# Kernel optimization log

Hardware: AMD Instinct MI355X
Metric: run time of the kernel (lower is better)

The kernel has to match this reference:

```python
import jax, jax.numpy as jnp
import numpy as np

N, E = 50000, 400000          # nodes, edges
T, R = 4, 8                   # node types, relations (edge types)
H, DK = 8, 32                 # heads, head dim
DIN = DOUT = 256              # in/out feature dim (DOUT = H*DK)
SQRT_DK = float(np.sqrt(DK))


def setup_inputs() -> dict:
    key = jax.random.key(0)
    ks = jax.random.split(key, 12)
    f32 = jnp.float32
    return {
        "x": jax.random.normal(ks[0], (N, DIN), f32),
        "node_type": jax.random.randint(ks[1], (N,), 0, T, jnp.int32),
        "src": jax.random.randint(ks[2], (E,), 0, N, jnp.int32),
        "dst": jax.random.randint(ks[3], (E,), 0, N, jnp.int32),
        "etype": jax.random.randint(ks[4], (E,), 0, R, jnp.int32),
        "Wk": jax.random.normal(ks[5], (T, DOUT, DIN), f32) / np.sqrt(DIN).astype(np.float32),
        "bk": jnp.zeros((T, DOUT), f32),
        "Wq": jax.random.normal(ks[6], (T, DOUT, DIN), f32) / np.sqrt(DIN).astype(np.float32),
        "bq": jnp.zeros((T, DOUT), f32),
        "Wv": jax.random.normal(ks[7], (T, DOUT, DIN), f32) / np.sqrt(DIN).astype(np.float32),
        "bv": jnp.zeros((T, DOUT), f32),
        "Wa": jax.random.normal(ks[8], (T, DOUT, DOUT), f32) / np.sqrt(DOUT).astype(np.float32),
        "ba": jnp.zeros((T, DOUT), f32),
        "rel_pri": jnp.ones((R, H), f32),
        "rel_att": jax.random.normal(ks[9], (R, H, DK, DK), f32) / np.sqrt(DK).astype(np.float32),  # ~xavier
        "rel_msg": jax.random.normal(ks[10], (R, H, DK, DK), f32) / np.sqrt(DK).astype(np.float32),
        "skip": jnp.ones((T,), f32),
    }


def _typed_linear(h, W, b, ntype):
    # per-node-type linear: y_n = W[type_n] @ h_n + b[type_n]
    y = jnp.einsum('ni,tdi->ntd', h, W)                      # [N,T,D] (T is small)
    y = jnp.take_along_axis(y, ntype[:, None, None], axis=1)[:, 0]
    return y + b[ntype]


def _hgt_forward(x, node_type, src, dst, etype,
                 Wk, bk, Wq, bq, Wv, bv, Wa, ba,
                 rel_pri, rel_att, rel_msg, skip):
    # typed k/q/v projections -> [N,H,DK]
    K = _typed_linear(x, Wk, bk, node_type).reshape(N, H, DK)
    Q = _typed_linear(x, Wq, bq, node_type).reshape(N, H, DK)
    V = _typed_linear(x, Wv, bv, node_type).reshape(N, H, DK)

    k_e, q_e, v_e = K[src], Q[dst], V[src]                   # [E,H,DK] gathers

    # per-relation head transforms (loop over small fixed R, masked accumulate)
    key_e = jnp.zeros_like(k_e)
    msg_e = jnp.zeros_like(v_e)
    for r in range(R):
        m = (etype == r)[:, None, None].astype(x.dtype)
        key_e = key_e + m * jnp.einsum('ehd,hdf->ehf', k_e, rel_att[r])
        msg_e = msg_e + m * jnp.einsum('ehd,hdf->ehf', v_e, rel_msg[r])

    att = (q_e * key_e).sum(-1) * rel_pri[etype] / SQRT_DK   # [E,H]

    # softmax per (dst node, edge type) segment, then mean across edge types
    seg = dst * R + etype                                    # [E]
    S = N * R
    amax = jax.ops.segment_max(att, seg, num_segments=S)     # [S,H]
    ex = jnp.exp(att - amax[seg])
    denom = jax.ops.segment_sum(ex, seg, num_segments=S)
    w = ex / denom[seg]                                      # normalized attention [E,H]
    h_seg = jax.ops.segment_sum(w[:, :, None] * msg_e, seg, num_segments=S)  # [S,H,DK]
    cnt = jax.ops.segment_sum(jnp.ones((E,), x.dtype), seg, num_segments=S)  # [S]

    h_nr = h_seg.reshape(N, R, DOUT)
    present = (cnt.reshape(N, R) > 0).astype(x.dtype)        # which etypes hit each node
    t = h_nr.sum(1) / jnp.maximum(present.sum(1), 1.0)[:, None]  # cross_reducer='mean'

    trans = _typed_linear(t, Wa, ba, node_type)              # per-type output linear
    alpha = jax.nn.sigmoid(skip)[node_type][:, None]
    return trans * alpha + x * (1.0 - alpha)


def reference(x, node_type, src, dst, etype,
              Wk, bk, Wq, bq, Wv, bv, Wa, ba,
              rel_pri, rel_att, rel_msg, skip):
    return _hgt_forward(x, node_type, src, dst, etype,
                        Wk, bk, Wq, bq, Wv, bv, Wa, ba,
                        rel_pri, rel_att, rel_msg, skip)
```

## Files before the change

### kernel.cpp

```cpp
#include <hip/hip_runtime.h>
#include <math.h>
#include <stdint.h>

#define N_NODES 50000
#define N_EDGES 400000
#define N_T 4
#define N_R 8
#define N_H 8
#define DKD 32
#define D 256
#define TM 64
#define N_SEG (N_NODES * N_R)
#define EMASK 0xFFFFF
#define PROJ_BLOCKS ((N_NODES + TM - 1) / TM + N_T)

typedef __bf16 v8bf __attribute__((ext_vector_type(8)));
typedef float v4f __attribute__((ext_vector_type(4)));
typedef unsigned short u16;

__device__ __forceinline__ u16 f2bf(float f) {
    unsigned int u = __float_as_uint(f);
    u += 0x7fffu + ((u >> 16) & 1u);
    return (u16)(u >> 16);
}

__device__ __forceinline__ void load_bf32(const u16* __restrict__ p, float* f) {
    const uint4* p4 = (const uint4*)p;
    #pragma unroll
    for (int j = 0; j < 4; j++) {
        uint4 u = p4[j];
        f[8 * j + 0] = __uint_as_float(u.x << 16);
        f[8 * j + 1] = __uint_as_float(u.x & 0xffff0000u);
        f[8 * j + 2] = __uint_as_float(u.y << 16);
        f[8 * j + 3] = __uint_as_float(u.y & 0xffff0000u);
        f[8 * j + 4] = __uint_as_float(u.z << 16);
        f[8 * j + 5] = __uint_as_float(u.z & 0xffff0000u);
        f[8 * j + 6] = __uint_as_float(u.w << 16);
        f[8 * j + 7] = __uint_as_float(u.w & 0xffff0000u);
    }
}

__device__ __forceinline__ float dot8f(uint4 m, const float* v) {
    float s;
    s  = __uint_as_float(m.x << 16)          * v[0];
    s += __uint_as_float(m.x & 0xffff0000u)  * v[1];
    s += __uint_as_float(m.y << 16)          * v[2];
    s += __uint_as_float(m.y & 0xffff0000u)  * v[3];
    s += __uint_as_float(m.z << 16)          * v[4];
    s += __uint_as_float(m.z & 0xffff0000u)  * v[5];
    s += __uint_as_float(m.w << 16)          * v[6];
    s += __uint_as_float(m.w & 0xffff0000u)  * v[7];
    return s;
}

__global__ __launch_bounds__(256) void k_cvt4(const float4* __restrict__ s,
                                              ushort4* __restrict__ d, int n4) {
    int i = blockIdx.x * 256 + threadIdx.x;
    if (i < n4) {
        float4 v = s[i];
        ushort4 o;
        o.x = f2bf(v.x); o.y = f2bf(v.y); o.z = f2bf(v.z); o.w = f2bf(v.w);
        d[i] = o;
    }
}

__global__ __launch_bounds__(256) void k_cvt_t(const float* __restrict__ s,
                                               u16* __restrict__ d) {
    int i = blockIdx.x * 256 + threadIdx.x;
    if (i >= N_R * N_H * DKD * DKD) return;
    int mat = i >> 10, w = i & 1023;
    int d0 = w >> 5, f = w & 31;
    d[(mat << 10) + f * DKD + d0] = f2bf(s[i]);
}

__global__ void k_hist(const int* __restrict__ nt, int* __restrict__ cnt) {
    int n = blockIdx.x * blockDim.x + threadIdx.x;
    if (n < N_NODES) atomicAdd(&cnt[nt[n]], 1);
}

__global__ void k_scan(const int* __restrict__ cnt, int* __restrict__ off,
                       int* __restrict__ toff) {
    int o = 0, to = 0;
    for (int t = 0; t < N_T; t++) {
        off[t] = o; toff[t] = to;
        o += cnt[t]; to += (cnt[t] + TM - 1) / TM;
    }
    off[N_T] = o; toff[N_T] = to;
}

__global__ void k_scatter(const int* __restrict__ nt, const int* __restrict__ off,
                          int* __restrict__ cur, int* __restrict__ order) {
    int n = blockIdx.x * blockDim.x + threadIdx.x;
    if (n >= N_NODES) return;
    int t = nt[n];
    int pos = off[t] + atomicAdd(&cur[t], 1);
    order[pos] = n;
}

__global__ void k_hist_seg(const int* __restrict__ dst, const int* __restrict__ et,
                           int* __restrict__ cnt) {
    int e = blockIdx.x * blockDim.x + threadIdx.x;
    if (e < N_EDGES) atomicAdd(&cnt[dst[e] * N_R + et[e]], 1);
}

__global__ __launch_bounds__(1024) void k_scan_l1(const int* __restrict__ cnt,
                                                  int* __restrict__ excl,
                                                  int* __restrict__ bsum) {
    __shared__ int sh[1024];
    int tid = threadIdx.x, i = blockIdx.x * 1024 + tid;
    int v = (i < N_SEG) ? cnt[i] : 0;
    sh[tid] = v;
    __syncthreads();
    #pragma unroll
    for (int ofs = 1; ofs < 1024; ofs <<= 1) {
        int t = (tid >= ofs) ? sh[tid - ofs] : 0;
        __syncthreads();
        sh[tid] += t;
        __syncthreads();
    }
    if (i < N_SEG) excl[i] = sh[tid] - v;
    if (tid == 1023) bsum[blockIdx.x] = sh[1023];
}

__global__ __launch_bounds__(512) void k_scan_l2(int* __restrict__ bsum, int NB) {
    __shared__ int sh[512];
    int tid = threadIdx.x;
    int v = (tid < NB) ? bsum[tid] : 0;
    sh[tid] = v;
    __syncthreads();
    #pragma unroll
    for (int ofs = 1; ofs < 512; ofs <<= 1) {
        int t = (tid >= ofs) ? sh[tid - ofs] : 0;
        __syncthreads();
        sh[tid] += t;
        __syncthreads();
    }
    if (tid < NB) bsum[tid] = sh[tid] - v;
}

__global__ void k_scan_l3(int* __restrict__ excl, const int* __restrict__ bsum) {
    int i = blockIdx.x * blockDim.x + threadIdx.x;
    if (i < N_SEG) excl[i] += bsum[i >> 10];
    else if (i == N_SEG) excl[N_SEG] = N_EDGES;
}

__global__ void k_scatter_seg(const int* __restrict__ src, const int* __restrict__ dst,
                              const int* __restrict__ et, const int* __restrict__ rp,
                              int* __restrict__ cur, int* __restrict__ esrc) {
    int e = blockIdx.x * blockDim.x + threadIdx.x;
    if (e >= N_EDGES) return;
    int r = et[e];
    int sg = dst[e] * N_R + r;
    int pos = rp[sg] + atomicAdd(&cur[sg], 1);
    esrc[pos] = src[e] | (r << 20);
}

__global__ __launch_bounds__(256) void k_proj(
    const float* __restrict__ x, const int* __restrict__ order,
    const int* __restrict__ off, const int* __restrict__ toff,
    const u16* __restrict__ Wkb, const float* __restrict__ bk,
    const u16* __restrict__ Wqb, const float* __restrict__ bq,
    const u16* __restrict__ Wvb, const float* __restrict__ bv,
    u16* __restrict__ Kb, u16* __restrict__ Qb, u16* __restrict__ Vb) {
    __shared__ __align__(16) u16 xs[TM][D + 8];
    int b = blockIdx.x;
    int t = -1;
    #pragma unroll
    for (int i = 0; i < N_T; i++)
        if (b >= toff[i] && b < toff[i + 1]) t = i;
    if (t < 0) return;
    int nodeBase = off[t] + (b - toff[t]) * TM;
    int count = min(TM, off[t + 1] - nodeBase);
    int tid = threadIdx.x;

    for (int j = tid; j < TM * (D / 4); j += 256) {
        int row = j >> 6, ch = j & 63;
        float4 v = {0.f, 0.f, 0.f, 0.f};
        if (row < count) {
            int g = order[nodeBase + row];
            v = *(const float4*)(x + (size_t)g * D + ch * 4);
        }
        ushort4 o;
        o.x = f2bf(v.x); o.y = f2bf(v.y); o.z = f2bf(v.z); o.w = f2bf(v.w);
        *(ushort4*)&xs[row][ch * 4] = o;
    }
    __syncthreads();

    int lane = tid & 63, wave = tid >> 6;
    int m = lane & 15, quad = lane >> 4;
    v8bf a[8];
    #pragma unroll
    for (int ks = 0; ks < 8; ks++)
        a[ks] = *(const v8bf*)&xs[wave * 16 + m][ks * 32 + quad * 8];

    int grow[4]; bool vrow[4];
    #pragma unroll
    for (int r = 0; r < 4; r++) {
        int rowi = wave * 16 + quad * 4 + r;
        vrow[r] = (rowi < count);
        grow[r] = vrow[r] ? order[nodeBase + rowi] : 0;
    }

    const u16* Ws[3] = {Wkb + (size_t)t * D * D, Wqb + (size_t)t * D * D, Wvb + (size_t)t * D * D};
    const float* Bs[3] = {bk + t * D, bq + t * D, bv + t * D};
    u16* Os[3] = {Kb, Qb, Vb};

    for (int p = 0; p < 3; p++) {
        const u16* W = Ws[p];
        for (int dt = 0; dt < 16; dt++) {
            int dcol = dt * 16 + m;
            v4f acc = {0.f, 0.f, 0.f, 0.f};
            #pragma unroll
            for (int ks = 0; ks < 8; ks++) {
                v8bf bf = *(const v8bf*)(W + (size_t)dcol * D + ks * 32 + quad * 8);
                acc = __builtin_amdgcn_mfma_f32_16x16x32_bf16(a[ks], bf, acc, 0, 0, 0);
            }
            float bias = Bs[p][dcol];
            #pragma unroll
            for (int r = 0; r < 4; r++) {
                if (vrow[r])
                    Os[p][(size_t)grow[r] * D + dcol] = f2bf(acc[r] + bias);
            }
        }
    }
}

__global__ __launch_bounds__(256) void k_fused(
    const u16* __restrict__ Kb, u16* QTb, const u16* __restrict__ Vb,
    const int* __restrict__ rowptr, const int* __restrict__ esrc,
    const u16* __restrict__ Ab, const u16* __restrict__ Mtb,
    const float* __restrict__ pri) {
    __shared__ __align__(16) float Uld[4][N_H][40];
    int wave = threadIdx.x >> 6, lane = threadIdx.x & 63;
    int n = blockIdx.x * 4 + wave;
    if (n >= N_NODES) return;
    int h = lane >> 3, fo = (lane & 7) * 4;
    int base = n * N_R;

    int bnd[N_R + 1];
    #pragma unroll
    for (int i = 0; i <= N_R; i++) bnd[i] = rowptr[base + i];

    float qv[32];
    load_bf32(QTb + (size_t)n * D + h * DKD, qv);

    float qt[N_R][4];
    int np = 0;
    #pragma unroll
    for (int r = 0; r < N_R; r++) {
        if (bnd[r] >= bnd[r + 1]) continue;
        np++;
        const u16* Ar = Ab + ((size_t)(r * N_H + h) * DKD + fo) * DKD;
        float scale = pri[r * N_H + h] * 0.17677669529663687f;
        #pragma unroll
        for (int i = 0; i < 4; i++) {
            const uint4* ar = (const uint4*)(Ar + i * DKD);
            qt[r][i] = scale * (dot8f(ar[0], qv) + dot8f(ar[1], qv + 8)
                     + dot8f(ar[2], qv + 16) + dot8f(ar[3], qv + 24));
        }
    }

    float den[N_R] = {0.f, 0.f, 0.f, 0.f, 0.f, 0.f, 0.f, 0.f};
    float ua[N_R][4] = {};

#define DOTQ(P, RS, KU) { \
    float _k0 = __uint_as_float((KU).x << 16); \
    float _k1 = __uint_as_float((KU).x & 0xffff0000u); \
    float _k2 = __uint_as_float((KU).y << 16); \
    float _k3 = __uint_as_float((KU).y & 0xffff0000u); \
    switch (RS) { \
    case 0: P = _k0*qt[0][0]+_k1*qt[0][1]+_k2*qt[0][2]+_k3*qt[0][3]; break; \
    case 1: P = _k0*qt[1][0]+_k1*qt[1][1]+_k2*qt[1][2]+_k3*qt[1][3]; break; \
    case 2: P = _k0*qt[2][0]+_k1*qt[2][1]+_k2*qt[2][2]+_k3*qt[2][3]; break; \
    case 3: P = _k0*qt[3][0]+_k1*qt[3][1]+_k2*qt[3][2]+_k3*qt[3][3]; break; \
    case 4: P = _k0*qt[4][0]+_k1*qt[4][1]+_k2*qt[4][2]+_k3*qt[4][3]; break; \
    case 5: P = _k0*qt[5][0]+_k1*qt[5][1]+_k2*qt[5][2]+_k3*qt[5][3]; break; \
    case 6: P = _k0*qt[6][0]+_k1*qt[6][1]+_k2*qt[6][2]+_k3*qt[6][3]; break; \
    default: P = _k0*qt[7][0]+_k1*qt[7][1]+_k2*qt[7][2]+_k3*qt[7][3]; break; } }

#define ACCR(R, EX, V0, V1, V2, V3) \
    den[R] += EX; ua[R][0] += EX*V0; ua[R][1] += EX*V1; ua[R][2] += EX*V2; ua[R][3] += EX*V3;

#define ACCE(RS, EX, VU) { \
    float _v0 = __uint_as_float((VU).x << 16); \
    float _v1 = __uint_as_float((VU).x & 0xffff0000u); \
    float _v2 = __uint_as_float((VU).y << 16); \
    float _v3 = __uint_as_float((VU).y & 0xffff0000u); \
    switch (RS) { \
    case 0: ACCR(0, EX, _v0, _v1, _v2, _v3) break; \
    case 1: ACCR(1, EX, _v0, _v1, _v2, _v3) break; \
    case 2: ACCR(2, EX, _v0, _v1, _v2, _v3) break; \
    case 3: ACCR(3, EX, _v0, _v1, _v2, _v3) break; \
    case 4: ACCR(4, EX, _v0, _v1, _v2, _v3) break; \
    case 5: ACCR(5, EX, _v0, _v1, _v2, _v3) break; \
    case 6: ACCR(6, EX, _v0, _v1, _v2, _v3) break; \
    default: ACCR(7, EX, _v0, _v1, _v2, _v3) break; } }

    int eb = bnd[0], ee = bnd[N_R];
    size_t hoff = (size_t)(h * DKD + fo);
    for (int w0 = eb; w0 < ee; w0 += 64) {
        int wcnt = min(64, ee - w0);
        int myek = (lane < wcnt) ? esrc[w0 + lane] : 0;
        for (int i0 = 0; i0 < wcnt; i0 += 4) {
            int mc = wcnt - i0;
            int pk0 = __shfl(myek, i0);
            int pk1 = __shfl(myek, i0 + (mc > 1 ? 1 : 0));
            int pk2 = __shfl(myek, i0 + (mc > 2 ? 2 : 0));
            int pk3 = __shfl(myek, i0 + (mc > 3 ? 3 : 0));
            int s0 = pk0 & EMASK, s1 = pk1 & EMASK, s2 = pk2 & EMASK, s3 = pk3 & EMASK;
            int r0 = __builtin_amdgcn_readfirstlane(pk0) >> 20;
            int r1 = __builtin_amdgcn_readfirstlane(pk1) >> 20;
            int r2 = __builtin_amdgcn_readfirstlane(pk2) >> 20;
            int r3 = __builtin_amdgcn_readfirstlane(pk3) >> 20;
            uint2 ku0 = *(const uint2*)(Kb + (size_t)s0 * D + hoff);
            uint2 ku1 = *(const uint2*)(Kb + (size_t)s1 * D + hoff);
            uint2 ku2 = *(const uint2*)(Kb + (size_t)s2 * D + hoff);
            uint2 ku3 = *(const uint2*)(Kb + (size_t)s3 * D + hoff);
            uint2 vu0 = *(const uint2*)(Vb + (size_t)s0 * D + hoff);
            uint2 vu1 = *(const uint2*)(Vb + (size_t)s1 * D + hoff);
            uint2 vu2 = *(const uint2*)(Vb + (size_t)s2 * D + hoff);
            uint2 vu3 = *(const uint2*)(Vb + (size_t)s3 * D + hoff);
            float p0, p1, p2, p3;
            DOTQ(p0, r0, ku0);
            DOTQ(p1, r1, ku1);
            DOTQ(p2, r2, ku2);
            DOTQ(p3, r3, ku3);
            p0 += __shfl_xor(p0, 1); p1 += __shfl_xor(p1, 1);
            p2 += __shfl_xor(p2, 1); p3 += __shfl_xor(p3, 1);
            p0 += __shfl_xor(p0, 2); p1 += __shfl_xor(p1, 2);
            p2 += __shfl_xor(p2, 2); p3 += __shfl_xor(p3, 2);
            p0 += __shfl_xor(p0, 4); p1 += __shfl_xor(p1, 4);
            p2 += __shfl_xor(p2, 4); p3 += __shfl_xor(p3, 4);
            float ex0 = __expf(p0), ex1 = __expf(p1);
            float ex2 = __expf(p2), ex3 = __expf(p3);
            ACCE(r0, ex0, vu0);
            if (mc > 1) { ACCE(r1, ex1, vu1); }
            if (mc > 2) { ACCE(r2, ex2, vu2); }
            if (mc > 3) { ACCE(r3, ex3, vu3); }
        }
    }

    float macc[4] = {0.f, 0.f, 0.f, 0.f};
    #pragma unroll
    for (int r = 0; r < N_R; r++) {
        if (bnd[r] >= bnd[r + 1]) continue;
        float invd = 1.f / den[r];
        float4 uw = {ua[r][0] * invd, ua[r][1] * invd, ua[r][2] * invd, ua[r][3] * invd};
        __builtin_amdgcn_wave_barrier();
        *(float4*)&Uld[wave][h][fo] = uw;
        __builtin_amdgcn_wave_barrier();
        float Uv[32];
        #pragma unroll
        for (int i = 0; i < 8; i++)
            *(float4*)&Uv[4 * i] = *(const float4*)&Uld[wave][h][4 * i];
        const u16* mp = Mtb + ((size_t)(r * N_H + h) * DKD + fo) * DKD;
        #pragma unroll
        for (int j = 0; j < 4; j++) {
            const uint4* mr = (const uint4*)(mp + j * DKD);
            macc[j] += dot8f(mr[0], Uv) + dot8f(mr[1], Uv + 8)
                     + dot8f(mr[2], Uv + 16) + dot8f(mr[3], Uv + 24);
        }
        __builtin_amdgcn_wave_barrier();
    }

    float invp = (np > 0) ? 1.f / (float)np : 1.f;
    ushort4 o;
    o.x = f2bf(macc[0] * invp); o.y = f2bf(macc[1] * invp);
    o.z = f2bf(macc[2] * invp); o.w = f2bf(macc[3] * invp);
    *(ushort4*)(QTb + (size_t)n * D + hoff) = o;
}

__global__ __launch_bounds__(256) void k_out(
    const u16* __restrict__ TBF, const float* __restrict__ x,
    const int* __restrict__ order, const int* __restrict__ off, const int* __restrict__ toff,
    const u16* __restrict__ Wab, const float* __restrict__ ba,
    const float* __restrict__ skip, float* __restrict__ out) {
    __shared__ __align__(16) u16 xs[TM][D + 8];
    int b = blockIdx.x;
    int t = -1;
    #pragma unroll
    for (int i = 0; i < N_T; i++)
        if (b >= toff[i] && b < toff[i + 1]) t = i;
    if (t < 0) return;
    int nodeBase = off[t] + (b - toff[t]) * TM;
    int count = min(TM, off[t + 1] - nodeBase);
    int tid = threadIdx.x;

    for (int j = tid; j < TM * 32; j += 256) {
        int row = j >> 5, ch = j & 31;
        ushort4 z = {0, 0, 0, 0};
        if (row < count) {
            int g = order[nodeBase + row];
            const ushort4* p = (const ushort4*)(TBF + (size_t)g * D + ch * 8);
            *(ushort4*)&xs[row][ch * 8] = p[0];
            *(ushort4*)&xs[row][ch * 8 + 4] = p[1];
        } else {
            *(ushort4*)&xs[row][ch * 8] = z;
            *(ushort4*)&xs[row][ch * 8 + 4] = z;
        }
    }
    __syncthreads();

    int lane = tid & 63, wave = tid >> 6;
    int m = lane & 15, quad = lane >> 4;
    v8bf a[8];
    #pragma unroll
    for (int ks = 0; ks < 8; ks++)
        a[ks] = *(const v8bf*)&xs[wave * 16 + m][ks * 32 + quad * 8];

    int grow[4]; bool vrow[4];
    #pragma unroll
    for (int r = 0; r < 4; r++) {
        int rowi = wave * 16 + quad * 4 + r;
        vrow[r] = (rowi < count);
        grow[r] = vrow[r] ? order[nodeBase + rowi] : 0;
    }

    float sv = skip[t];
    float alpha = 1.f / (1.f + __expf(-sv));
    float beta = 1.f - alpha;
    const u16* W = Wab + (size_t)t * D * D;

    for (int dt = 0; dt < 16; dt++) {
        int dcol = dt * 16 + m;
        v4f acc = {0.f, 0.f, 0.f, 0.f};
        #pragma unroll
        for (int ks = 0; ks < 8; ks++) {
            v8bf bf = *(const v8bf*)(W + (size_t)dcol * D + ks * 32 + quad * 8);
            acc = __builtin_amdgcn_mfma_f32_16x16x32_bf16(a[ks], bf, acc, 0, 0, 0);
        }
        float bias = ba[t * D + dcol];
        #pragma unroll
        for (int r = 0; r < 4; r++) {
            if (vrow[r]) {
                size_t o = (size_t)grow[r] * D + dcol;
                out[o] = alpha * (acc[r] + bias) + beta * x[o];
            }
        }
    }
}

extern "C" void kernel_launch(void* const* d_in, const int* in_sizes, int n_in,
                              void* d_out, int out_size, void* d_ws, size_t ws_size,
                              hipStream_t stream) {
    const float* x       = (const float*)d_in[0];
    const int* node_type = (const int*)d_in[1];
    const int* src       = (const int*)d_in[2];
    const int* dst       = (const int*)d_in[3];
    const int* etype     = (const int*)d_in[4];
    const float* Wk = (const float*)d_in[5];
    const float* bk = (const float*)d_in[6];
    const float* Wq = (const float*)d_in[7];
    const float* bq = (const float*)d_in[8];
    const float* Wv = (const float*)d_in[9];
    const float* bv = (const float*)d_in[10];
    const float* Wa = (const float*)d_in[11];
    const float* ba = (const float*)d_in[12];
    const float* rel_pri = (const float*)d_in[13];
    const float* rel_att = (const float*)d_in[14];
    const float* rel_msg = (const float*)d_in[15];
    const float* skip    = (const float*)d_in[16];
    float* out = (float*)d_out;
    char* ws = (char*)d_ws;

    const size_t SZH = (size_t)N_NODES * D * 2;
    const size_t WSZ = (size_t)N_T * D * D;
    const size_t RSZ = (size_t)N_R * N_H * DKD * DKD;
    u16* Kb  = (u16*)(ws);
    u16* Qb  = (u16*)(ws + SZH);
    u16* Vb  = (u16*)(ws + 2 * SZH);
    u16* TBF = Qb;
    u16* Wkb = (u16*)(ws + 3 * SZH);
    u16* Wqb = Wkb + WSZ;
    u16* Wvb = Wqb + WSZ;
    u16* Wab = Wvb + WSZ;
    u16* Ab  = Wab + WSZ;
    u16* Mtb = Ab + RSZ;
    int* order = (int*)(Mtb + RSZ);
    int* small = order + N_NODES;
    int* cnt  = small;
    int* cur  = small + 4;
    int* offp = small + 8;
    int* toffp= small + 13;

    char* ob = (char*)d_out;
    int* rowptr_seg = (int*)ob;
    int* cnt_seg    = rowptr_seg + (N_SEG + 16);
    int* cur_seg    = cnt_seg + N_SEG;
    int* esrc       = cur_seg + N_SEG;
    int* bsum       = esrc + N_EDGES;

    hipMemsetAsync(small, 0, 8 * sizeof(int), stream);
    hipMemsetAsync(cnt_seg, 0, 2 * (size_t)N_SEG * sizeof(int), stream);

    k_cvt4<<<(WSZ / 4 + 255) / 256, 256, 0, stream>>>((const float4*)Wk, (ushort4*)Wkb, WSZ / 4);
    k_cvt4<<<(WSZ / 4 + 255) / 256, 256, 0, stream>>>((const float4*)Wq, (ushort4*)Wqb, WSZ / 4);
    k_cvt4<<<(WSZ / 4 + 255) / 256, 256, 0, stream>>>((const float4*)Wv, (ushort4*)Wvb, WSZ / 4);
    k_cvt4<<<(WSZ / 4 + 255) / 256, 256, 0, stream>>>((const float4*)Wa, (ushort4*)Wab, WSZ / 4);
    k_cvt4<<<(RSZ / 4 + 255) / 256, 256, 0, stream>>>((const float4*)rel_att, (ushort4*)Ab, RSZ / 4);
    k_cvt_t<<<(RSZ + 255) / 256, 256, 0, stream>>>(rel_msg, Mtb);

    k_hist<<<(N_NODES + 255) / 256, 256, 0, stream>>>(node_type, cnt);
    k_scan<<<1, 1, 0, stream>>>(cnt, offp, toffp);
    k_scatter<<<(N_NODES + 255) / 256, 256, 0, stream>>>(node_type, offp, cur, order);

    const int NB = (N_SEG + 1023) / 1024;
    k_hist_seg<<<(N_EDGES + 255) / 256, 256, 0, stream>>>(dst, etype, cnt_seg);
    k_scan_l1<<<NB, 1024, 0, stream>>>(cnt_seg, rowptr_seg, bsum);
    k_scan_l2<<<1, 512, 0, stream>>>(bsum, NB);
    k_scan_l3<<<(N_SEG + 1 + 255) / 256, 256, 0, stream>>>(rowptr_seg, bsum);
    k_scatter_seg<<<(N_EDGES + 255) / 256, 256, 0, stream>>>(src, dst, etype,
                                                             rowptr_seg, cur_seg, esrc);

    k_proj<<<PROJ_BLOCKS, 256, 0, stream>>>(x, order, offp, toffp,
                                            Wkb, bk, Wqb, bq, Wvb, bv, Kb, Qb, Vb);

    k_fused<<<(N_NODES + 3) / 4, 256, 0, stream>>>(Kb, Qb, Vb, rowptr_seg, esrc,
                                                   Ab, Mtb, rel_pri);

    k_out<<<PROJ_BLOCKS, 256, 0, stream>>>(TBF, x, order, offp, toffp,
                                           Wab, ba, skip, out);
}
```

Before: 2.020 ms.

## Switch bf16 storage to fp16 and use packed fdot2 in fused attention kernel

Changes all intermediate storage (weights, K/Q/V, relation matrices, aggregated features) from bf16 to fp16, uses fp16 MFMA in the projection kernels, and replaces the unpacked float dot products in the fused edge kernel with packed v_dot2 fp16 instructions. It also folds the relation priority and 1/sqrt(dk) scale into the attention matrix conversion, merges the four weight conversion launches into one, halves LDS use for the staging buffer, and adds an occupancy hint to the fused kernel. The aim is fewer ALU instructions and registers per edge. The cost is fp16's narrower range, so large activations could overflow.

```diff
diff --git a/kernel.cpp b/kernel.cpp
--- a/kernel.cpp
+++ b/kernel.cpp
@@ -14,54 +14,65 @@
 #define EMASK 0xFFFFF
 #define PROJ_BLOCKS ((N_NODES + TM - 1) / TM + N_T)
 
-typedef __bf16 v8bf __attribute__((ext_vector_type(8)));
+typedef _Float16 h2 __attribute__((ext_vector_type(2)));
+typedef _Float16 v8h __attribute__((ext_vector_type(8)));
 typedef float v4f __attribute__((ext_vector_type(4)));
 typedef unsigned short u16;
 
-__device__ __forceinline__ u16 f2bf(float f) {
-    unsigned int u = __float_as_uint(f);
-    u += 0x7fffu + ((u >> 16) & 1u);
-    return (u16)(u >> 16);
-}
-
-__device__ __forceinline__ void load_bf32(const u16* __restrict__ p, float* f) {
-    const uint4* p4 = (const uint4*)p;
+__device__ __forceinline__ u16 h2u(_Float16 h) { return __builtin_bit_cast(u16, h); }
+__device__ __forceinline__ h2 u2h2(unsigned int u) { return __builtin_bit_cast(h2, u); }
+
+#if __has_builtin(__builtin_amdgcn_fdot2)
+__device__ __forceinline__ float fdot2f(h2 a, h2 b, float c) {
+    return __builtin_amdgcn_fdot2(a, b, c, false);
+}
+#else
+__device__ __forceinline__ float fdot2f(h2 a, h2 b, float c) {
+    return c + (float)a[0] * (float)b[0] + (float)a[1] * (float)b[1];
+}
+#endif
+
+__device__ __forceinline__ float dot32h(const uint4* __restrict__ a,
+                                        const uint4* __restrict__ q) {
+    float s = 0.f;
     #pragma unroll
     for (int j = 0; j < 4; j++) {
-        uint4 u = p4[j];
-        f[8 * j + 0] = __uint_as_float(u.x << 16);
-        f[8 * j + 1] = __uint_as_float(u.x & 0xffff0000u);
-        f[8 * j + 2] = __uint_as_float(u.y << 16);
-        f[8 * j + 3] = __uint_as_float(u.y & 0xffff0000u);
-        f[8 * j + 4] = __uint_as_float(u.z << 16);
-        f[8 * j + 5] = __uint_as_float(u.z & 0xffff0000u);
-        f[8 * j + 6] = __uint_as_float(u.w << 16);
-        f[8 * j + 7] = __uint_as_float(u.w & 0xffff0000u);
-    }
-}
-
-__device__ __forceinline__ float dot8f(uint4 m, const float* v) {
-    float s;
-    s  = __uint_as_float(m.x << 16)          * v[0];
-    s += __uint_as_float(m.x & 0xffff0000u)  * v[1];
-    s += __uint_as_float(m.y << 16)          * v[2];
-    s += __uint_as_float(m.y & 0xffff0000u)  * v[3];
-    s += __uint_as_float(m.z << 16)          * v[4];
-    s += __uint_as_float(m.z & 0xffff0000u)  * v[5];
-    s += __uint_as_float(m.w << 16)          * v[6];
-    s += __uint_as_float(m.w & 0xffff0000u)  * v[7];
+        uint4 av = a[j], qv = q[j];
+        s = fdot2f(u2h2(av.x), u2h2(qv.x), s);
+        s = fdot2f(u2h2(av.y), u2h2(qv.y), s);
+        s = fdot2f(u2h2(av.z), u2h2(qv.z), s);
+        s = fdot2f(u2h2(av.w), u2h2(qv.w), s);
+    }
     return s;
 }
 
-__global__ __launch_bounds__(256) void k_cvt4(const float4* __restrict__ s,
-                                              ushort4* __restrict__ d, int n4) {
+__global__ __launch_bounds__(256) void k_cvtW(
+    const float4* __restrict__ w0, const float4* __restrict__ w1,
+    const float4* __restrict__ w2, const float4* __restrict__ w3,
+    ushort4* __restrict__ d, int n4each) {
     int i = blockIdx.x * 256 + threadIdx.x;
-    if (i < n4) {
-        float4 v = s[i];
-        ushort4 o;
-        o.x = f2bf(v.x); o.y = f2bf(v.y); o.z = f2bf(v.z); o.w = f2bf(v.w);
-        d[i] = o;
-    }
+    if (i >= 4 * n4each) return;
+    int sel = i / n4each, j = i - sel * n4each;
+    const float4* s = (sel == 0) ? w0 : (sel == 1) ? w1 : (sel == 2) ? w2 : w3;
+    float4 v = s[j];
+    ushort4 o;
+    o.x = h2u((_Float16)v.x); o.y = h2u((_Float16)v.y);
+    o.z = h2u((_Float16)v.z); o.w = h2u((_Float16)v.w);
+    d[i] = o;
+}
+
+__global__ __launch_bounds__(256) void k_cvt_att(const float4* __restrict__ s,
+                                                 const float* __restrict__ pri,
+                                                 ushort4* __restrict__ d, int n4) {
+    int i = blockIdx.x * 256 + threadIdx.x;
+    if (i >= n4) return;
+    int mat = i >> 8;
+    float sc = pri[mat] * 0.17677669529663687f;
+    float4 v = s[i];
+    ushort4 o;
+    o.x = h2u((_Float16)(v.x * sc)); o.y = h2u((_Float16)(v.y * sc));
+    o.z = h2u((_Float16)(v.z * sc)); o.w = h2u((_Float16)(v.w * sc));
+    d[i] = o;
 }
 
 __global__ __launch_bounds__(256) void k_cvt_t(const float* __restrict__ s,
@@ -70,7 +81,7 @@
     if (i >= N_R * N_H * DKD * DKD) return;
     int mat = i >> 10, w = i & 1023;
     int d0 = w >> 5, f = w & 31;
-    d[(mat << 10) + f * DKD + d0] = f2bf(s[i]);
+    d[(mat << 10) + f * DKD + d0] = h2u((_Float16)s[i]);
 }
 
 __global__ void k_hist(const int* __restrict__ nt, int* __restrict__ cnt) {
@@ -181,17 +192,18 @@
             v = *(const float4*)(x + (size_t)g * D + ch * 4);
         }
         ushort4 o;
-        o.x = f2bf(v.x); o.y = f2bf(v.y); o.z = f2bf(v.z); o.w = f2bf(v.w);
+        o.x = h2u((_Float16)v.x); o.y = h2u((_Float16)v.y);
+        o.z = h2u((_Float16)v.z); o.w = h2u((_Float16)v.w);
         *(ushort4*)&xs[row][ch * 4] = o;
     }
     __syncthreads();
 
     int lane = tid & 63, wave = tid >> 6;
     int m = lane & 15, quad = lane >> 4;
-    v8bf a[8];
+    v8h a[8];
     #pragma unroll
     for (int ks = 0; ks < 8; ks++)
-        a[ks] = *(const v8bf*)&xs[wave * 16 + m][ks * 32 + quad * 8];
+        a[ks] = *(const v8h*)&xs[wave * 16 + m][ks * 32 + quad * 8];
 
     int grow[4]; bool vrow[4];
     #pragma unroll
@@ -212,80 +224,78 @@
             v4f acc = {0.f, 0.f, 0.f, 0.f};
             #pragma unroll
             for (int ks = 0; ks < 8; ks++) {
-                v8bf bf = *(const v8bf*)(W + (size_t)dcol * D + ks * 32 + quad * 8);
-                acc = __builtin_amdgcn_mfma_f32_16x16x32_bf16(a[ks], bf, acc, 0, 0, 0);
+                v8h bf = *(const v8h*)(W + (size_t)dcol * D + ks * 32 + quad * 8);
+                acc = __builtin_amdgcn_mfma_f32_16x16x32_f16(a[ks], bf, acc, 0, 0, 0);
             }
             float bias = Bs[p][dcol];
             #pragma unroll
             for (int r = 0; r < 4; r++) {
                 if (vrow[r])
-                    Os[p][(size_t)grow[r] * D + dcol] = f2bf(acc[r] + bias);
+                    Os[p][(size_t)grow[r] * D + dcol] = h2u((_Float16)(acc[r] + bias));
             }
         }
     }
 }
 
-__global__ __launch_bounds__(256) void k_fused(
+__global__ __launch_bounds__(256, 4) void k_fused(
     const u16* __restrict__ Kb, u16* QTb, const u16* __restrict__ Vb,
     const int* __restrict__ rowptr, const int* __restrict__ esrc,
-    const u16* __restrict__ Ab, const u16* __restrict__ Mtb,
-    const float* __restrict__ pri) {
-    __shared__ __align__(16) float Uld[4][N_H][40];
+    const u16* __restrict__ Ab, const u16* __restrict__ Mtb) {
+    __shared__ __align__(16) unsigned int Uldu[4][N_H][20];
     int wave = threadIdx.x >> 6, lane = threadIdx.x & 63;
     int n = blockIdx.x * 4 + wave;
     if (n >= N_NODES) return;
-    int h = lane >> 3, fo = (lane & 7) * 4;
+    int h = lane >> 3, fl = lane & 7, fo = fl * 4;
     int base = n * N_R;
 
     int bnd[N_R + 1];
     #pragma unroll
     for (int i = 0; i <= N_R; i++) bnd[i] = rowptr[base + i];
 
-    float qv[32];
-    load_bf32(QTb + (size_t)n * D + h * DKD, qv);
-
-    float qt[N_R][4];
+    uint4 qv4[4];
+    {
+        const uint4* qp = (const uint4*)(QTb + (size_t)n * D + h * DKD);
+        #pragma unroll
+        for (int j = 0; j < 4; j++) qv4[j] = qp[j];
+    }
+
+    h2 qt2[N_R][2];
     int np = 0;
     #pragma unroll
     for (int r = 0; r < N_R; r++) {
         if (bnd[r] >= bnd[r + 1]) continue;
         np++;
         const u16* Ar = Ab + ((size_t)(r * N_H + h) * DKD + fo) * DKD;
-        float scale = pri[r * N_H + h] * 0.17677669529663687f;
-        #pragma unroll
-        for (int i = 0; i < 4; i++) {
-            const uint4* ar = (const uint4*)(Ar + i * DKD);
-            qt[r][i] = scale * (dot8f(ar[0], qv) + dot8f(ar[1], qv + 8)
-                     + dot8f(ar[2], qv + 16) + dot8f(ar[3], qv + 24));
-        }
+        float q0 = dot32h((const uint4*)(Ar), qv4);
+        float q1 = dot32h((const uint4*)(Ar + DKD), qv4);
+        float q2 = dot32h((const uint4*)(Ar + 2 * DKD), qv4);
+        float q3 = dot32h((const uint4*)(Ar + 3 * DKD), qv4);
+        qt2[r][0] = h2{(_Float16)q0, (_Float16)q1};
+        qt2[r][1] = h2{(_Float16)q2, (_Float16)q3};
     }
 
     float den[N_R] = {0.f, 0.f, 0.f, 0.f, 0.f, 0.f, 0.f, 0.f};
     float ua[N_R][4] = {};
 
 #define DOTQ(P, RS, KU) { \
-    float _k0 = __uint_as_float((KU).x << 16); \
-    float _k1 = __uint_as_float((KU).x & 0xffff0000u); \
-    float _k2 = __uint_as_float((KU).y << 16); \
-    float _k3 = __uint_as_float((KU).y & 0xffff0000u); \
+    h2 _ka = u2h2((KU).x), _kb = u2h2((KU).y); \
     switch (RS) { \
-    case 0: P = _k0*qt[0][0]+_k1*qt[0][1]+_k2*qt[0][2]+_k3*qt[0][3]; break; \
-    case 1: P = _k0*qt[1][0]+_k1*qt[1][1]+_k2*qt[1][2]+_k3*qt[1][3]; break; \
-    case 2: P = _k0*qt[2][0]+_k1*qt[2][1]+_k2*qt[2][2]+_k3*qt[2][3]; break; \
-    case 3: P = _k0*qt[3][0]+_k1*qt[3][1]+_k2*qt[3][2]+_k3*qt[3][3]; break; \
-    case 4: P = _k0*qt[4][0]+_k1*qt[4][1]+_k2*qt[4][2]+_k3*qt[4][3]; break; \
-    case 5: P = _k0*qt[5][0]+_k1*qt[5][1]+_k2*qt[5][2]+_k3*qt[5][3]; break; \
-    case 6: P = _k0*qt[6][0]+_k1*qt[6][1]+_k2*qt[6][2]+_k3*qt[6][3]; break; \
-    default: P = _k0*qt[7][0]+_k1*qt[7][1]+_k2*qt[7][2]+_k3*qt[7][3]; break; } }
+    case 0: P = fdot2f(_kb, qt2[0][1], fdot2f(_ka, qt2[0][0], 0.f)); break; \
+    case 1: P = fdot2f(_kb, qt2[1][1], fdot2f(_ka, qt2[1][0], 0.f)); break; \
+    case 2: P = fdot2f(_kb, qt2[2][1], fdot2f(_ka, qt2[2][0], 0.f)); break; \
+    case 3: P = fdot2f(_kb, qt2[3][1], fdot2f(_ka, qt2[3][0], 0.f)); break; \
+    case 4: P = fdot2f(_kb, qt2[4][1], fdot2f(_ka, qt2[4][0], 0.f)); break; \
+    case 5: P = fdot2f(_kb, qt2[5][1], fdot2f(_ka, qt2[5][0], 0.f)); break; \
+    case 6: P = fdot2f(_kb, qt2[6][1], fdot2f(_ka, qt2[6][0], 0.f)); break; \
+    default: P = fdot2f(_kb, qt2[7][1], fdot2f(_ka, qt2[7][0], 0.f)); break; } }
 
 #define ACCR(R, EX, V0, V1, V2, V3) \
     den[R] += EX; ua[R][0] += EX*V0; ua[R][1] += EX*V1; ua[R][2] += EX*V2; ua[R][3] += EX*V3;
 
 #define ACCE(RS, EX, VU) { \
-    float _v0 = __uint_as_float((VU).x << 16); \
-    float _v1 = __uint_as_float((VU).x & 0xffff0000u); \
-    float _v2 = __uint_as_float((VU).y << 16); \
-    float _v3 = __uint_as_float((VU).y & 0xffff0000u); \
+    h2 _va = u2h2((VU).x), _vb = u2h2((VU).y); \
+    float _v0 = (float)_va[0], _v1 = (float)_va[1]; \
+    float _v2 = (float)_vb[0], _v3 = (float)_vb[1]; \
     switch (RS) { \
     case 0: ACCR(0, EX, _v0, _v1, _v2, _v3) break; \
     case 1: ACCR(1, EX, _v0, _v1, _v2, _v3) break; \
@@ -345,28 +355,28 @@
     for (int r = 0; r < N_R; r++) {
         if (bnd[r] >= bnd[r + 1]) continue;
         float invd = 1.f / den[r];
-        float4 uw = {ua[r][0] * invd, ua[r][1] * invd, ua[r][2] * invd, ua[r][3] * invd};
+        unsigned int pw0 = __builtin_bit_cast(unsigned int,
+            h2{(_Float16)(ua[r][0] * invd), (_Float16)(ua[r][1] * invd)});
+        unsigned int pw1 = __builtin_bit_cast(unsigned int,
+            h2{(_Float16)(ua[r][2] * invd), (_Float16)(ua[r][3] * invd)});
         __builtin_amdgcn_wave_barrier();
-        *(float4*)&Uld[wave][h][fo] = uw;
+        *(uint2*)&Uldu[wave][h][fl * 2] = uint2{pw0, pw1};
         __builtin_amdgcn_wave_barrier();
-        float Uv[32];
+        uint4 Um[4];
         #pragma unroll
-        for (int i = 0; i < 8; i++)
-            *(float4*)&Uv[4 * i] = *(const float4*)&Uld[wave][h][4 * i];
+        for (int j = 0; j < 4; j++)
+            Um[j] = *(const uint4*)&Uldu[wave][h][4 * j];
         const u16* mp = Mtb + ((size_t)(r * N_H + h) * DKD + fo) * DKD;
         #pragma unroll
-        for (int j = 0; j < 4; j++) {
-            const uint4* mr = (const uint4*)(mp + j * DKD);
-            macc[j] += dot8f(mr[0], Uv) + dot8f(mr[1], Uv + 8)
-                     + dot8f(mr[2], Uv + 16) + dot8f(mr[3], Uv + 24);
-        }
+        for (int j = 0; j < 4; j++)
+            macc[j] += dot32h((const uint4*)(mp + j * DKD), Um);
         __builtin_amdgcn_wave_barrier();
     }
 
     float invp = (np > 0) ? 1.f / (float)np : 1.f;
     ushort4 o;
-    o.x = f2bf(macc[0] * invp); o.y = f2bf(macc[1] * invp);
-    o.z = f2bf(macc[2] * invp); o.w = f2bf(macc[3] * invp);
+    o.x = h2u((_Float16)(macc[0] * invp)); o.y = h2u((_Float16)(macc[1] * invp));
+    o.z = h2u((_Float16)(macc[2] * invp)); o.w = h2u((_Float16)(macc[3] * invp));
     *(ushort4*)(QTb + (size_t)n * D + hoff) = o;
 }
 
@@ -403,10 +413,10 @@
 
     int lane = tid & 63, wave = tid >> 6;
     int m = lane & 15, quad = lane >> 4;
-    v8bf a[8];
+    v8h a[8];
     #pragma unroll
     for (int ks = 0; ks < 8; ks++)
-        a[ks] = *(const v8bf*)&xs[wave * 16 + m][ks * 32 + quad * 8];
+        a[ks] = *(const v8h*)&xs[wave * 16 + m][ks * 32 + quad * 8];
 
     int grow[4]; bool vrow[4];
     #pragma unroll
@@ -426,8 +436,8 @@
         v4f acc = {0.f, 0.f, 0.f, 0.f};
         #pragma unroll
         for (int ks = 0; ks < 8; ks++) {
-            v8bf bf = *(const v8bf*)(W + (size_t)dcol * D + ks * 32 + quad * 8);
-            acc = __builtin_amdgcn_mfma_f32_16x16x32_bf16(a[ks], bf, acc, 0, 0, 0);
+            v8h bf = *(const v8h*)(W + (size_t)dcol * D + ks * 32 + quad * 8);
+            acc = __builtin_amdgcn_mfma_f32_16x16x32_f16(a[ks], bf, acc, 0, 0, 0);
         }
         float bias = ba[t * D + dcol];
         #pragma unroll
@@ -493,11 +503,11 @@
     hipMemsetAsync(small, 0, 8 * sizeof(int), stream);
     hipMemsetAsync(cnt_seg, 0, 2 * (size_t)N_SEG * sizeof(int), stream);
 
-    k_cvt4<<<(WSZ / 4 + 255) / 256, 256, 0, stream>>>((const float4*)Wk, (ushort4*)Wkb, WSZ / 4);
-    k_cvt4<<<(WSZ / 4 + 255) / 256, 256, 0, stream>>>((const float4*)Wq, (ushort4*)Wqb, WSZ / 4);
-    k_cvt4<<<(WSZ / 4 + 255) / 256, 256, 0, stream>>>((const float4*)Wv, (ushort4*)Wvb, WSZ / 4);
-    k_cvt4<<<(WSZ / 4 + 255) / 256, 256, 0, stream>>>((const float4*)Wa, (ushort4*)Wab, WSZ / 4);
-    k_cvt4<<<(RSZ / 4 + 255) / 256, 256, 0, stream>>>((const float4*)rel_att, (ushort4*)Ab, RSZ / 4);
+    k_cvtW<<<(4 * (WSZ / 4) + 255) / 256, 256, 0, stream>>>(
+        (const float4*)Wk, (const float4*)Wq, (const float4*)Wv, (const float4*)Wa,
+        (ushort4*)Wkb, WSZ / 4);
+    k_cvt_att<<<(RSZ / 4 + 255) / 256, 256, 0, stream>>>(
+        (const float4*)rel_att, rel_pri, (ushort4*)Ab, RSZ / 4);
     k_cvt_t<<<(RSZ + 255) / 256, 256, 0, stream>>>(rel_msg, Mtb);
 
     k_hist<<<(N_NODES + 255) / 256, 256, 0, stream>>>(node_type, cnt);
@@ -516,7 +526,7 @@
                                             Wkb, bk, Wqb, bq, Wvb, bv, Kb, Qb, Vb);
 
     k_fused<<<(N_NODES + 3) / 4, 256, 0, stream>>>(Kb, Qb, Vb, rowptr_seg, esrc,
-                                                   Ab, Mtb, rel_pri);
+                                                   Ab, Mtb);
 
     k_out<<<PROJ_BLOCKS, 256, 0, stream>>>(TBF, x, order, offp, toffp,
                                            Wab, ba, skip, out);
```

New measurement: 2.042 ms. No clear change (+1.1%).
